# Kernel tuning notes

Hardware: AMD Instinct MI355X
Metric: run time of the kernel (lower is better)

## Reference

```python
import jax, jax.numpy as jnp
import numpy as np

B, IN_CH, OUT_CH = 4, 64, 128
N_HIGH, N_LOW = 163842, 40962
GROUPS, EPS, SLOPE = 4, 1e-5, 0.2


def setup_inputs() -> dict:
    key = jax.random.key(0)
    ks = jax.random.split(key, 6)
    x = jax.random.normal(ks[0], (B, IN_CH, N_HIGH), jnp.float32)
    pool_neigh = jax.random.randint(ks[1], (N_LOW * 7,), 0, N_HIGH, dtype=jnp.int32)
    conv_neigh = jax.random.randint(ks[2], (N_LOW * 7,), 0, N_LOW, dtype=jnp.int32)
    W1 = jax.random.normal(ks[3], (OUT_CH, 7 * IN_CH), jnp.float32) / np.float32(np.sqrt(7 * IN_CH))
    b1 = jnp.zeros((OUT_CH,), jnp.float32)
    W2 = jax.random.normal(ks[4], (OUT_CH, 7 * OUT_CH), jnp.float32) / np.float32(np.sqrt(7 * OUT_CH))
    b2 = jnp.zeros((OUT_CH,), jnp.float32)
    return dict(x=x, pool_neigh=pool_neigh, conv_neigh=conv_neigh,
                W1=W1, b1=b1, gn1_w=jnp.ones((OUT_CH,), jnp.float32), gn1_b=jnp.zeros((OUT_CH,), jnp.float32),
                W2=W2, b2=b2, gn2_w=jnp.ones((OUT_CH,), jnp.float32), gn2_b=jnp.zeros((OUT_CH,), jnp.float32))


def _mean_pool(x, pool_neigh):
    # x: (B, C, N_high); pool_neigh: (N_low*7,) -> (B, C, N_low)
    g = x[:, :, pool_neigh].reshape(x.shape[0], x.shape[1], -1, 7)
    return g.mean(axis=-1)


def _onering_conv(x, neigh, W, b):
    # x: (B, C, N); neigh: (N*7,); W: (O, 7*C). Torch Linear over gathered
    # (N*7, C).view(N, 7*C): neighbor-major, channel-minor concatenation.
    Bb, C, N = x.shape
    feat = x[:, :, neigh].reshape(Bb, C, N, 7)            # (B, C, N, 7)
    feat = jnp.transpose(feat, (0, 2, 3, 1)).reshape(Bb, N, 7 * C)  # (B, N, 7C)
    out = jnp.einsum('bnf,of->bno', feat, W) + b          # (B, N, O)
    return jnp.transpose(out, (0, 2, 1))                  # (B, O, N)


def _group_norm(x, w, b):
    # x: (B, C, N), normalize per (group, sample) over (C//G, N)
    Bb, C, N = x.shape
    xg = x.reshape(Bb, GROUPS, C // GROUPS, N)
    mu = xg.mean(axis=(2, 3), keepdims=True)
    var = ((xg - mu) ** 2).mean(axis=(2, 3), keepdims=True)
    xn = ((xg - mu) * jax.lax.rsqrt(var + EPS)).reshape(Bb, C, N)
    return xn * w[None, :, None] + b[None, :, None]


def _leaky_relu(x):
    return jnp.where(x >= 0, x, SLOPE * x)


def reference(x, pool_neigh, conv_neigh, W1, b1, gn1_w, gn1_b, W2, b2, gn2_w, gn2_b):
    h = _mean_pool(x, pool_neigh)
    h = _leaky_relu(_group_norm(_onering_conv(h, conv_neigh, W1, b1), gn1_w, gn1_b))
    h = _leaky_relu(_group_norm(_onering_conv(h, conv_neigh, W2, b2), gn2_w, gn2_b))
    return h
```

## Files before the change

### kernel.cpp

```cpp
#include <hip/hip_runtime.h>

#define B_SZ 4
#define IN_CH 64
#define OUT_CH 128
#define NHI 163842
#define NLO 40962
#define EPS_GN 1e-5f
#define SLOPE 0.2f

typedef __attribute__((ext_vector_type(8))) short short8;
typedef __attribute__((ext_vector_type(16))) float f32x16;

__device__ inline ushort f2bf(float f) {
    union { float f; unsigned u; } v; v.f = f;
    unsigned r = v.u + 0x7FFF + ((v.u >> 16) & 1);
    return (ushort)(r >> 16);
}
__device__ inline float bf2f(ushort h) {
    union { unsigned u; float f; } v; v.u = ((unsigned)h) << 16;
    return v.f;
}

__global__ void k_transpose_x(const float* __restrict__ x, ushort* __restrict__ xT) {
    __shared__ float t[64][65];
    const int b   = blockIdx.y;
    const int n0  = blockIdx.x * 64;
    const int tid = threadIdx.x;
    const int nq  = tid & 15;
    const int c0  = tid >> 4;
    const bool full = (n0 + 64) <= NHI;
    if (full) {
#pragma unroll
        for (int r = 0; r < 4; ++r) {
            int c = c0 + r * 16;
            float4 v = *(const float4*)&x[((long)b * IN_CH + c) * NHI + n0 + nq * 4];
            t[c][nq * 4 + 0] = v.x; t[c][nq * 4 + 1] = v.y;
            t[c][nq * 4 + 2] = v.z; t[c][nq * 4 + 3] = v.w;
        }
    } else {
        for (int r = 0; r < 4; ++r) {
            int c = c0 + r * 16;
            for (int e = 0; e < 4; ++e) {
                int n = n0 + nq * 4 + e;
                t[c][nq * 4 + e] = (n < NHI) ? x[((long)b * IN_CH + c) * NHI + n] : 0.f;
            }
        }
    }
    __syncthreads();
    const int n  = tid >> 2;
    const int cc = (tid & 3) * 16;
    if (n0 + n < NHI) {
        short8 o0, o1;
#pragma unroll
        for (int e = 0; e < 8; ++e) {
            o0[e] = (short)f2bf(t[cc + e][n]);
            o1[e] = (short)f2bf(t[cc + 8 + e][n]);
        }
        ushort* p = &xT[((long)b * NHI + n0 + n) * 64 + cc];
        *(short8*)p = o0;
        *(short8*)(p + 8) = o1;
    }
}

__global__ void k_prep_w(const float* __restrict__ W, ushort* __restrict__ Wb, int K) {
    int i = blockIdx.x * 256 + threadIdx.x;
    if (i >= K * 128) return;
    int k = i / 128, o = i % 128;
    int step = k >> 6, kk = k & 63, kg = kk >> 3, e = kk & 7;
    Wb[(((long)(step * 8 + kg) * 128 + o) * 8) + e] = f2bf(W[(long)o * K + k]);
}

__global__ void k_pool(const ushort* __restrict__ xT, const int* __restrict__ pn,
                       ushort* __restrict__ h1) {
    long t = (long)blockIdx.x * 256 + threadIdx.x;
    const long total = (long)B_SZ * NLO * 8;
    if (t >= total) return;
    int  cq = (int)(t & 7);
    long bn = t >> 3;
    int  n  = (int)(bn % NLO);
    int  b  = (int)(bn / NLO);
    float acc[8] = {};
#pragma unroll
    for (int j = 0; j < 7; ++j) {
        int idx = pn[n * 7 + j];
        short8 v = *(const short8*)&xT[((long)b * NHI + idx) * 64 + cq * 8];
#pragma unroll
        for (int e = 0; e < 8; ++e) acc[e] += bf2f((ushort)v[e]);
    }
    short8 o;
#pragma unroll
    for (int e = 0; e < 8; ++e) o[e] = (short)f2bf(acc[e] * (1.f / 7.f));
    *(short8*)&h1[bn * 64 + cq * 8] = o;
}

__device__ inline int aidx(int kg, int nn) {
    return (kg * 128 + (nn ^ (kg << 1))) * 8;
}

template <int CIN>
__global__ __launch_bounds__(512, 4)
void k_conv_mfma(const ushort* __restrict__ src, const int* __restrict__ nbr,
                 const ushort* __restrict__ Wb, const float* __restrict__ bias,
                 ushort* __restrict__ out, float* __restrict__ part) {
    constexpr int K = 7 * CIN;
    constexpr int NSTEP = K / 64;
    __shared__ ushort Asm[2][8192];
    __shared__ ushort Bsm[2][8192];
    __shared__ float  red[8][4];

    const int b    = blockIdx.y;
    const int n0   = blockIdx.x * 128;
    const int tid  = threadIdx.x;
    const int lane = tid & 63;
    const int wave = tid >> 6;
    const int wr   = wave >> 1, wc = wave & 1;

    const int s_nn = tid >> 2;
    const int s_kq = tid & 3;
    int nrow = n0 + s_nn; if (nrow >= NLO) nrow = NLO - 1;
    const int* nbr_row = &nbr[nrow * 7];

    f32x16 acc0 = {}, acc1 = {};
    const long srcb = (long)b * NLO * CIN;

    const int arow  = wr * 32 + (lane & 31);
    const int bcol0 = wc * 64 + (lane & 31);
    const int khalf = lane >> 5;

    short8 ar[4][2];
    short8 w0, w1;

    auto loadA = [&](int t, short8* d) {
        int j, cb;
        if (CIN == 64) { j = t; cb = 0; }
        else           { j = t >> 1; cb = (t & 1) * 64; }
        const ushort* sp = &src[srcb + (long)nbr_row[j] * CIN + cb + s_kq * 8];
        d[0] = *(const short8*)sp;
        d[1] = *(const short8*)(sp + 32);
    };

    {
        const ushort* wp = &Wb[tid * 16];
        w0 = *(const short8*)wp;
        w1 = *(const short8*)(wp + 8);
    }
#pragma unroll
    for (int t = 0; t < 4; ++t)
        if (t < NSTEP) loadA(t, ar[t]);

#pragma unroll
    for (int step = 0; step < NSTEP; ++step) {
        const int cur = step & 1;
        const int slot = step & 3;
        *(short8*)&Asm[cur][aidx(s_kq,     s_nn)] = ar[slot][0];
        *(short8*)&Asm[cur][aidx(s_kq + 4, s_nn)] = ar[slot][1];
        *(short8*)&Bsm[cur][tid * 16]     = w0;
        *(short8*)&Bsm[cur][tid * 16 + 8] = w1;
        __syncthreads();
        if (step + 4 < NSTEP) loadA(step + 4, ar[slot]);
        if (step + 1 < NSTEP) {
            const ushort* wp = &Wb[(long)(step + 1) * 8192 + tid * 16];
            w0 = *(const short8*)wp;
            w1 = *(const short8*)(wp + 8);
        }
#pragma unroll
        for (int kh = 0; kh < 4; ++kh) {
            int kg = 2 * kh + khalf;
            short8 af  = *(const short8*)&Asm[cur][aidx(kg, arow)];
            short8 bf0 = *(const short8*)&Bsm[cur][(kg * 128 + bcol0) * 8];
            short8 bf1 = *(const short8*)&Bsm[cur][(kg * 128 + bcol0 + 32) * 8];
            acc0 = __builtin_amdgcn_mfma_f32_32x32x16_bf16(af, bf0, acc0, 0, 0, 0);
            acc1 = __builtin_amdgcn_mfma_f32_32x32x16_bf16(af, bf1, acc1, 0, 0, 0);
        }
    }

    const float bias0 = bias[wc * 64 + (lane & 31)];
    const float bias1 = bias[wc * 64 + 32 + (lane & 31)];
    float s0 = 0.f, q0 = 0.f, s1 = 0.f, q1 = 0.f;
#pragma unroll
    for (int r = 0; r < 16; ++r) {
        int rrow = (r & 3) + 8 * (r >> 2) + 4 * khalf + wr * 32;
        int n = n0 + rrow;
        float v0 = acc0[r] + bias0;
        float v1 = acc1[r] + bias1;
        if (n < NLO) {
            long o = ((long)b * NLO + n) * 128 + wc * 64 + (lane & 31);
            out[o]      = f2bf(v0);
            out[o + 32] = f2bf(v1);
            s0 += v0; q0 += v0 * v0;
            s1 += v1; q1 += v1 * v1;
        }
    }
#pragma unroll
    for (int off = 32; off > 0; off >>= 1) {
        s0 += __shfl_down(s0, off); q0 += __shfl_down(q0, off);
        s1 += __shfl_down(s1, off); q1 += __shfl_down(q1, off);
    }
    if (lane == 0) { red[wave][0] = s0; red[wave][1] = q0; red[wave][2] = s1; red[wave][3] = q1; }
    __syncthreads();
    if (tid < 8) {
        int g = tid >> 1, isq = tid & 1;
        int wcg = g >> 1, ct = g & 1;
        float v = 0.f;
#pragma unroll
        for (int w = 0; w < 4; ++w) v += red[w * 2 + wcg][ct * 2 + isq];
        part[(((long)b * gridDim.x + blockIdx.x) * 4 + g) * 2 + isq] = v;
    }
}

__global__ void k_finalize(const float* __restrict__ part, int nblk,
                           const float* __restrict__ w, const float* __restrict__ bb,
                           float* __restrict__ scale, float* __restrict__ shift) {
    const int b = blockIdx.x >> 2, g = blockIdx.x & 3;
    const int tid = threadIdx.x;
    float s = 0.f, ss = 0.f;
    for (int k = tid; k < nblk; k += 256) {
        s  += part[(((long)b * nblk + k) * 4 + g) * 2 + 0];
        ss += part[(((long)b * nblk + k) * 4 + g) * 2 + 1];
    }
#pragma unroll
    for (int off = 32; off > 0; off >>= 1) {
        s += __shfl_down(s, off); ss += __shfl_down(ss, off);
    }
    __shared__ float red[8];
    __shared__ float fin[2];
    const int wave = tid >> 6, lane = tid & 63;
    if (lane == 0) { red[wave * 2] = s; red[wave * 2 + 1] = ss; }
    __syncthreads();
    if (tid == 0) {
        float as = red[0] + red[2] + red[4] + red[6];
        float aq = red[1] + red[3] + red[5] + red[7];
        const float cnt = 32.f * NLO;
        float mu  = as / cnt;
        float var = aq / cnt - mu * mu;
        fin[0] = mu; fin[1] = rsqrtf(var + EPS_GN);
    }
    __syncthreads();
    if (tid < 32) {
        int c = g * 32 + tid;
        float sc = fin[1] * w[c];
        scale[b * 128 + c] = sc;
        shift[b * 128 + c] = bb[c] - fin[0] * sc;
    }
}

__global__ void k_gnapply(const ushort* __restrict__ y, const float* __restrict__ sc,
                          const float* __restrict__ sh, ushort* __restrict__ yp) {
    long t = (long)blockIdx.x * 256 + threadIdx.x;
    const long total = (long)B_SZ * NLO * 16;
    if (t >= total) return;
    int  c8 = (int)(t & 15);
    long bn = t >> 4;
    int  b  = (int)(bn / NLO);
    short8 v = *(const short8*)&y[bn * 128 + c8 * 8];
    short8 o;
#pragma unroll
    for (int e = 0; e < 8; ++e) {
        int c = c8 * 8 + e;
        float f = bf2f((ushort)v[e]) * sc[b * 128 + c] + sh[b * 128 + c];
        f = fmaxf(f, SLOPE * f);
        o[e] = (short)f2bf(f);
    }
    *(short8*)&yp[bn * 128 + c8 * 8] = o;
}

__global__ void k_output(const ushort* __restrict__ y2, const float* __restrict__ scale,
                         const float* __restrict__ shift, float* __restrict__ out) {
    __shared__ float t[32][129];
    const int b   = blockIdx.y;
    const int n0  = blockIdx.x * 32;
    const int tid = threadIdx.x;
    const float* scb = &scale[b * 128];
    const float* shb = &shift[b * 128];
    const int c8 = (tid & 15) * 8;
#pragma unroll
    for (int r = 0; r < 2; ++r) {
        int nn = (tid >> 4) + r * 16;
        int n  = n0 + nn;
        if (n < NLO) {
            short8 v = *(const short8*)&y2[((long)b * NLO + n) * 128 + c8];
#pragma unroll
            for (int e = 0; e < 8; ++e) {
                int c = c8 + e;
                float f = bf2f((ushort)v[e]) * scb[c] + shb[c];
                t[nn][c] = fmaxf(f, SLOPE * f);
            }
        } else {
#pragma unroll
            for (int e = 0; e < 8; ++e) t[nn][c8 + e] = 0.f;
        }
    }
    __syncthreads();
    const int n4 = (tid & 7) * 4;
    const bool full = (n0 + 32) <= NLO;
#pragma unroll
    for (int r = 0; r < 4; ++r) {
        int c = (tid >> 3) + r * 32;
        long o = ((long)b * 128 + c) * NLO + n0 + n4;
        if (full) {
            float2 v0 = make_float2(t[n4][c], t[n4 + 1][c]);
            float2 v1 = make_float2(t[n4 + 2][c], t[n4 + 3][c]);
            *(float2*)&out[o]     = v0;
            *(float2*)&out[o + 2] = v1;
        } else {
            for (int e = 0; e < 4; ++e)
                if (n0 + n4 + e < NLO) out[o + e] = t[n4 + e][c];
        }
    }
}

extern "C" void kernel_launch(void* const* d_in, const int* in_sizes, int n_in,
                              void* d_out, int out_size, void* d_ws, size_t ws_size,
                              hipStream_t stream) {
    const float* x   = (const float*)d_in[0];
    const int*   pn  = (const int*)d_in[1];
    const int*   cn  = (const int*)d_in[2];
    const float* W1  = (const float*)d_in[3];
    const float* b1  = (const float*)d_in[4];
    const float* g1w = (const float*)d_in[5];
    const float* g1b = (const float*)d_in[6];
    const float* W2  = (const float*)d_in[7];
    const float* b2  = (const float*)d_in[8];
    const float* g2w = (const float*)d_in[9];
    const float* g2b = (const float*)d_in[10];
    float* out = (float*)d_out;
    char*  base = (char*)d_ws;

    ushort* xT  = (ushort*)(base + 0);
    ushort* y1  = (ushort*)(base + 0);
    ushort* y1p = (ushort*)(base + 44000000);
    ushort* h1  = (ushort*)(base + 88000000);
    ushort* y2  = (ushort*)(base + 110000000);
    ushort* wb1 = (ushort*)(base + 152000000);
    ushort* wb2 = (ushort*)(base + 152200000);
    float*  p1  = (float*)(base + 152500000);
    float*  p2  = (float*)(base + 152600000);
    float*  sc1 = (float*)(base + 152700000);
    float*  sh1 = sc1 + 512;
    float*  sc2 = (float*)(base + 152710000);
    float*  sh2 = sc2 + 512;

    const int NBLK = (NLO + 127) / 128;

    k_transpose_x<<<dim3((NHI + 63) / 64, B_SZ), 256, 0, stream>>>(x, xT);
    k_prep_w<<<(448 * 128 + 255) / 256, 256, 0, stream>>>(W1, wb1, 448);
    k_prep_w<<<(896 * 128 + 255) / 256, 256, 0, stream>>>(W2, wb2, 896);
    k_pool<<<(int)(((long)B_SZ * NLO * 8 + 255) / 256), 256, 0, stream>>>(xT, pn, h1);
    k_conv_mfma<64><<<dim3(NBLK, B_SZ), 512, 0, stream>>>(h1, cn, wb1, b1, y1, p1);
    k_finalize<<<16, 256, 0, stream>>>(p1, NBLK, g1w, g1b, sc1, sh1);
    k_gnapply<<<(int)(((long)B_SZ * NLO * 16 + 255) / 256), 256, 0, stream>>>(y1, sc1, sh1, y1p);
    k_conv_mfma<128><<<dim3(NBLK, B_SZ), 512, 0, stream>>>(y1p, cn, wb2, b2, y2, p2);
    k_finalize<<<16, 256, 0, stream>>>(p2, NBLK, g2w, g2b, sc2, sh2);
    k_output<<<dim3((NLO + 31) / 32, B_SZ), 256, 0, stream>>>(y2, sc2, sh2, out);
}
```

Before: 247.6 us.

## Halve conv K-step, raise occupancy, stream weights into LDS via global_load_lds

The one-ring conv MFMA kernel now walks K in steps of 32 instead of 64, which halves the A and B shared-memory buffers. The launch-bounds occupancy hint rises from 4 to 6 blocks. Weights are copied from global memory straight into LDS with global_load_lds rather than staged through registers, and the weight prep kernel is given a matching layout. The four-deep register prefetch of gathered A rows becomes a single-step prefetch, and neighbor indices are kept in registers. The goal is to hide gather latency through more resident waves and fewer registers, at the cost of more barriers per tile and a shallower prefetch.

```diff
diff --git a/kernel.cpp b/kernel.cpp
--- a/kernel.cpp
+++ b/kernel.cpp
@@ -19,6 +19,12 @@
 __device__ inline float bf2f(ushort h) {
     union { unsigned u; float f; } v; v.u = ((unsigned)h) << 16;
     return v.f;
+}
+
+__device__ inline void glds16(const ushort* g, ushort* l) {
+    typedef __attribute__((address_space(1))) const void gv;
+    typedef __attribute__((address_space(3))) void lv;
+    __builtin_amdgcn_global_load_lds((gv*)g, (lv*)l, 16, 0, 0);
 }
 
 __global__ void k_transpose_x(const float* __restrict__ x, ushort* __restrict__ xT) {
@@ -66,8 +72,7 @@
     int i = blockIdx.x * 256 + threadIdx.x;
     if (i >= K * 128) return;
     int k = i / 128, o = i % 128;
-    int step = k >> 6, kk = k & 63, kg = kk >> 3, e = kk & 7;
-    Wb[(((long)(step * 8 + kg) * 128 + o) * 8) + e] = f2bf(W[(long)o * K + k]);
+    Wb[(long)(k >> 3) * 1024 + o * 8 + (k & 7)] = f2bf(W[(long)o * K + k]);
 }
 
 __global__ void k_pool(const ushort* __restrict__ xT, const int* __restrict__ pn,
@@ -98,14 +103,13 @@
 }
 
 template <int CIN>
-__global__ __launch_bounds__(512, 4)
+__global__ __launch_bounds__(512, 6)
 void k_conv_mfma(const ushort* __restrict__ src, const int* __restrict__ nbr,
                  const ushort* __restrict__ Wb, const float* __restrict__ bias,
                  ushort* __restrict__ out, float* __restrict__ part) {
-    constexpr int K = 7 * CIN;
-    constexpr int NSTEP = K / 64;
-    __shared__ ushort Asm[2][8192];
-    __shared__ ushort Bsm[2][8192];
+    constexpr int NSTEP = 7 * CIN / 32;
+    __shared__ ushort Asm[2][4096];
+    __shared__ ushort Bsm[2][4096];
     __shared__ float  red[8][4];
 
     const int b    = blockIdx.y;
@@ -114,68 +118,53 @@
     const int lane = tid & 63;
     const int wave = tid >> 6;
     const int wr   = wave >> 1, wc = wave & 1;
+    const int l31  = lane & 31;
+    const int khalf = lane >> 5;
 
     const int s_nn = tid >> 2;
     const int s_kq = tid & 3;
     int nrow = n0 + s_nn; if (nrow >= NLO) nrow = NLO - 1;
-    const int* nbr_row = &nbr[nrow * 7];
-
+    int nb[7];
+#pragma unroll
+    for (int j = 0; j < 7; ++j) nb[j] = nbr[nrow * 7 + j];
+
+    const long srcb = (long)b * NLO * CIN;
     f32x16 acc0 = {}, acc1 = {};
-    const long srcb = (long)b * NLO * CIN;
-
-    const int arow  = wr * 32 + (lane & 31);
-    const int bcol0 = wc * 64 + (lane & 31);
-    const int khalf = lane >> 5;
-
-    short8 ar[4][2];
-    short8 w0, w1;
-
-    auto loadA = [&](int t, short8* d) {
+    const int arow = wr * 32 + l31;
+    const int bcol = wc * 64 + l31;
+    short8 a;
+
+    auto loadA = [&](int t) {
         int j, cb;
-        if (CIN == 64) { j = t; cb = 0; }
-        else           { j = t >> 1; cb = (t & 1) * 64; }
-        const ushort* sp = &src[srcb + (long)nbr_row[j] * CIN + cb + s_kq * 8];
-        d[0] = *(const short8*)sp;
-        d[1] = *(const short8*)(sp + 32);
+        if (CIN == 64) { j = t >> 1; cb = (t & 1) * 32; }
+        else           { j = t >> 2; cb = (t & 3) * 32; }
+        a = *(const short8*)&src[srcb + (long)nb[j] * CIN + cb + s_kq * 8];
     };
 
-    {
-        const ushort* wp = &Wb[tid * 16];
-        w0 = *(const short8*)wp;
-        w1 = *(const short8*)(wp + 8);
-    }
-#pragma unroll
-    for (int t = 0; t < 4; ++t)
-        if (t < NSTEP) loadA(t, ar[t]);
-
-#pragma unroll
-    for (int step = 0; step < NSTEP; ++step) {
-        const int cur = step & 1;
-        const int slot = step & 3;
-        *(short8*)&Asm[cur][aidx(s_kq,     s_nn)] = ar[slot][0];
-        *(short8*)&Asm[cur][aidx(s_kq + 4, s_nn)] = ar[slot][1];
-        *(short8*)&Bsm[cur][tid * 16]     = w0;
-        *(short8*)&Bsm[cur][tid * 16 + 8] = w1;
+    glds16(&Wb[tid * 8], &Bsm[0][tid * 8]);
+    loadA(0);
+
+    for (int t = 0; t < NSTEP; ++t) {
+        const int cur = t & 1;
+        *(short8*)&Asm[cur][aidx(s_kq, s_nn)] = a;
         __syncthreads();
-        if (step + 4 < NSTEP) loadA(step + 4, ar[slot]);
-        if (step + 1 < NSTEP) {
-            const ushort* wp = &Wb[(long)(step + 1) * 8192 + tid * 16];
-            w0 = *(const short8*)wp;
-            w1 = *(const short8*)(wp + 8);
-        }
-#pragma unroll
-        for (int kh = 0; kh < 4; ++kh) {
-            int kg = 2 * kh + khalf;
-            short8 af  = *(const short8*)&Asm[cur][aidx(kg, arow)];
-            short8 bf0 = *(const short8*)&Bsm[cur][(kg * 128 + bcol0) * 8];
-            short8 bf1 = *(const short8*)&Bsm[cur][(kg * 128 + bcol0 + 32) * 8];
-            acc0 = __builtin_amdgcn_mfma_f32_32x32x16_bf16(af, bf0, acc0, 0, 0, 0);
-            acc1 = __builtin_amdgcn_mfma_f32_32x32x16_bf16(af, bf1, acc1, 0, 0, 0);
-        }
-    }
-
-    const float bias0 = bias[wc * 64 + (lane & 31)];
-    const float bias1 = bias[wc * 64 + 32 + (lane & 31)];
+        if (t + 1 < NSTEP) {
+            glds16(&Wb[(long)(t + 1) * 4096 + tid * 8], &Bsm[cur ^ 1][tid * 8]);
+            loadA(t + 1);
+        }
+#pragma unroll
+        for (int kh = 0; kh < 2; ++kh) {
+            const int kg = 2 * kh + khalf;
+            short8 af = *(const short8*)&Asm[cur][aidx(kg, arow)];
+            short8 b0 = *(const short8*)&Bsm[cur][(kg * 128 + bcol) * 8];
+            short8 b1 = *(const short8*)&Bsm[cur][(kg * 128 + bcol + 32) * 8];
+            acc0 = __builtin_amdgcn_mfma_f32_32x32x16_bf16(af, b0, acc0, 0, 0, 0);
+            acc1 = __builtin_amdgcn_mfma_f32_32x32x16_bf16(af, b1, acc1, 0, 0, 0);
+        }
+    }
+
+    const float bias0 = bias[wc * 64 + l31];
+    const float bias1 = bias[wc * 64 + 32 + l31];
     float s0 = 0.f, q0 = 0.f, s1 = 0.f, q1 = 0.f;
 #pragma unroll
     for (int r = 0; r < 16; ++r) {
@@ -184,7 +173,7 @@
         float v0 = acc0[r] + bias0;
         float v1 = acc1[r] + bias1;
         if (n < NLO) {
-            long o = ((long)b * NLO + n) * 128 + wc * 64 + (lane & 31);
+            long o = ((long)b * NLO + n) * 128 + wc * 64 + l31;
             out[o]      = f2bf(v0);
             out[o + 32] = f2bf(v1);
             s0 += v0; q0 += v0 * v0;
```

After: 243.4 us. Within noise of the previous version (-1.7%).
